# Optimization experiments

Hardware: AMD Instinct MI355X
Metric: run time of the kernel (lower is better)

Reference implementation:

```python
import jax, jax.numpy as jnp
import numpy as np

PATCH = 4   # patch_size
TOPK = 2    # top_k

B, H, W, C = 4, 128, 128, 256
FF, E = 1024, 4


def setup_inputs() -> dict:
    key = jax.random.key(0)
    k1, k2, k3, k4 = jax.random.split(key, 4)
    x = jax.random.normal(k1, (B, H, W, C), dtype=jnp.float32)
    Wg = jax.random.normal(k2, (E, C), dtype=jnp.float32) * 0.01   # router gate (std=0.01 init)
    lim1 = (6.0 / (C + FF)) ** 0.5                                  # xavier_uniform bounds
    W1 = jax.random.uniform(k3, (E, FF, C), minval=-lim1, maxval=lim1, dtype=jnp.float32)
    b1 = jnp.zeros((E, FF), dtype=jnp.float32)
    W2 = jax.random.uniform(k4, (E, C, FF), minval=-lim1, maxval=lim1, dtype=jnp.float32)
    b2 = jnp.zeros((E, C), dtype=jnp.float32)
    return {"x": x, "Wg": Wg, "W1": W1, "b1": b1, "W2": W2, "b2": b2}


def reference(x, Wg, W1, b1, W2, b2):
    Bs, Hs, Ws, Cs = x.shape
    Es = Wg.shape[0]
    ph = pw = PATCH
    nh, nw = Hs // ph, Ws // pw
    P = nh * nw
    # [B, nh, ph, nw, pw, C]
    xp = x.reshape(Bs, nh, ph, nw, pw, Cs)
    # --- router: per-patch avg pool + linear gate ---
    means = xp.mean(axis=(2, 4))                                  # [B, nh, nw, C]
    logits = jnp.einsum('bhwc,ec->bhwe', means, Wg).reshape(Bs, P, Es)
    probs = jax.nn.softmax(logits, axis=-1)
    w, idx = jax.lax.top_k(probs, TOPK)                           # [B, P, K]
    w = w / (w.sum(axis=-1, keepdims=True) + 1e-9)
    # dense combine weights per expert: [B, P, E]
    comb = (jax.nn.one_hot(idx, Es, dtype=w.dtype) * w[..., None]).sum(axis=-2)
    # --- expert dispatch/combine over patch tokens ---
    tokens = xp.transpose(0, 1, 3, 2, 4, 5).reshape(Bs, P, ph * pw, Cs)  # [B,P,T,C]
    out = jnp.zeros_like(tokens)
    for e in range(Es):  # small fixed expert set
        h = jax.nn.gelu(jnp.einsum('bptc,fc->bptf', tokens, W1[e]) + b1[e],
                        approximate=False)
        y = jnp.einsum('bptf,cf->bptc', h, W2[e]) + b2[e]
        out = out + comb[:, :, e, None, None] * y
    # reassemble patches -> [B, H, W, C]
    out = out.reshape(Bs, nh, nw, ph, pw, Cs).transpose(0, 1, 3, 2, 4, 5)
    return out.reshape(Bs, Hs, Ws, Cs)
```

## Files before the change

kernel.cpp:

```cpp
#include <hip/hip_runtime.h>
#include <hip/hip_bf16.h>
#include <cstdint>

#define NB 4
#define NH 128
#define NW 128
#define NC 256
#define NFF 1024
#define NE 4
#define NPATCH 4096
#define NPAIR 16
#define PPB 4
#define BM 64
#define FFC 256

typedef __attribute__((ext_vector_type(8))) short short8;
typedef __attribute__((ext_vector_type(8))) unsigned short ushort8;
typedef __attribute__((ext_vector_type(4))) float f32x4;

__device__ __forceinline__ unsigned short f2b(float f) {
  union { float f; uint32_t u; } v; v.f = f;
  uint32_t u = v.u + 0x7FFFu + ((v.u >> 16) & 1u);
  return (unsigned short)(u >> 16);
}

__device__ __forceinline__ float gelu_f(float v) {
  float u = v * v;
  float t = __builtin_fmaf(u, 0.044715f, 1.0f) * v;
  float e = __builtin_amdgcn_exp2f(t * -2.3022083f);
  return v * __builtin_amdgcn_rcpf(1.0f + e);
}

__device__ __forceinline__ void bar_lgkm() {
  asm volatile("s_waitcnt lgkmcnt(0)" ::: "memory");
  __builtin_amdgcn_s_barrier();
}

__global__ __launch_bounds__(256) void convert_kernel(
    const float* __restrict__ W1, const float* __restrict__ W2,
    unsigned short* __restrict__ W1b, unsigned short* __restrict__ W2b,
    int* __restrict__ cnt, int n) {
  int i = blockIdx.x * blockDim.x + threadIdx.x;
  if (i < NPAIR) cnt[i] = 0;
  if (i < n) {
    W1b[i] = f2b(W1[i]);
    W2b[i] = f2b(W2[i]);
  }
}

__global__ __launch_bounds__(256) void router_kernel(
    const float* __restrict__ x, const float* __restrict__ Wg,
    int* __restrict__ cnt, int* __restrict__ plist, float2* __restrict__ wlist) {
  int p = blockIdx.x;
  int b = p >> 10, pi = p & 1023;
  int phi = pi >> 5, pwi = pi & 31;
  int c = threadIdx.x;

  const float* base = x + (((size_t)(b * NH + phi * 4) * NW) + pwi * 4) * NC + c;
  float s = 0.f;
#pragma unroll
  for (int i = 0; i < 4; i++)
#pragma unroll
    for (int j = 0; j < 4; j++)
      s += base[(i * NW + j) * NC];
  float mean = s * (1.f / 16.f);

  __shared__ float m_lds[NC];
  __shared__ double logit_lds[NE];
  m_lds[c] = mean;
  __syncthreads();

  int wid = c >> 6, lane = c & 63;
  {
    const float* wg = Wg + wid * NC;
    double acc = 0.0;
#pragma unroll
    for (int q = 0; q < 4; q++)
      acc += (double)m_lds[lane + q * 64] * (double)wg[lane + q * 64];
    for (int off = 32; off; off >>= 1) acc += __shfl_down(acc, off);
    if (lane == 0) logit_lds[wid] = acc;
  }
  __syncthreads();

  if (c == 0) {
    double l[NE], pp[NE];
    double mx = -1e300;
#pragma unroll
    for (int i = 0; i < NE; i++) { l[i] = logit_lds[i]; mx = fmax(mx, l[i]); }
    double sum = 0.0;
#pragma unroll
    for (int i = 0; i < NE; i++) { pp[i] = exp(l[i] - mx); sum += pp[i]; }
#pragma unroll
    for (int i = 0; i < NE; i++) pp[i] /= sum;
    int i1 = 0; double p1 = pp[0];
    for (int i = 1; i < NE; i++) if (pp[i] > p1) { p1 = pp[i]; i1 = i; }
    int i2 = -1; double p2 = -1.0;
    for (int i = 0; i < NE; i++) {
      if (i == i1) continue;
      if (pp[i] > p2) { p2 = pp[i]; i2 = i; }
    }
    double den = p1 + p2 + 1e-9;
    float w1 = (float)(p1 / den), w2 = (float)(p2 / den);
    int pr = i1 * NE + i2;
    int pos = atomicAdd(&cnt[pr], 1);
    plist[pr * NPATCH + pos] = p;
    wlist[pr * NPATCH + pos] = make_float2(w1, w2);
  }
}

__global__ __launch_bounds__(256, 2) void ffn_kernel(
    const float* __restrict__ x, const float* __restrict__ b1,
    const float* __restrict__ b2, const unsigned short* __restrict__ W1b,
    const unsigned short* __restrict__ W2b, const int* __restrict__ cnt,
    const int* __restrict__ plist, const float2* __restrict__ wlist,
    float* __restrict__ out) {
  __shared__ unsigned short Xl[BM * NC];
  __shared__ unsigned short Hl[BM * FFC];

  int bid = blockIdx.x;
  int pr = bid & 15;
  int e1 = pr >> 2, e2 = pr & 3;
  int tile = bid >> 4;
  int n = cnt[pr];
  int pbase = tile * PPB;
  if (pbase >= n) return;

  int tid = threadIdx.x, lane = tid & 63, wid = tid >> 6;
  int l15 = lane & 15;
  int kgrp = (lane >> 4) * 8;

  const int*    pl = plist + pr * NPATCH + pbase;
  const float2* wl = wlist + pr * NPATCH + pbase;

  float wvA[PPB], wvB[PPB];
#pragma unroll
  for (int q = 0; q < PPB; q++) {
    if (pbase + q < n) { float2 w = wl[q]; wvA[q] = w.x; wvB[q] = w.y; }
    else { wvA[q] = 0.f; wvB[q] = 0.f; }
  }

  {
    int r  = tid >> 2;
    int c0 = (tid & 3) * 64;
    int pid = (pbase + (r >> 4) < n) ? pl[r >> 4] : -1;
    int t = r & 15;
    if (pid >= 0) {
      int b = pid >> 10, pi = pid & 1023;
      int phi = pi >> 5, pwi = pi & 31;
      const float* src =
          x + (((size_t)(b * NH + phi * 4 + (t >> 2)) * NW) + pwi * 4 + (t & 3)) * NC + c0;
#pragma unroll
      for (int q = 0; q < 8; q++) {
        float4 v0 = *reinterpret_cast<const float4*>(src + q * 8);
        float4 v1 = *reinterpret_cast<const float4*>(src + q * 8 + 4);
        ushort8 h;
        h[0] = f2b(v0.x); h[1] = f2b(v0.y); h[2] = f2b(v0.z); h[3] = f2b(v0.w);
        h[4] = f2b(v1.x); h[5] = f2b(v1.y); h[6] = f2b(v1.z); h[7] = f2b(v1.w);
        int boff = (r * 512 + (c0 + q * 8) * 2) ^ ((r & 7) << 4);
        *reinterpret_cast<ushort8*>((char*)Xl + boff) = h;
      }
    } else {
      ushort8 h = (ushort8)0;
#pragma unroll
      for (int q = 0; q < 8; q++) {
        int boff = (r * 512 + (c0 + q * 8) * 2) ^ ((r & 7) << 4);
        *reinterpret_cast<ushort8*>((char*)Xl + boff) = h;
      }
    }
  }
  bar_lgkm();

  const unsigned short* W1A = W1b + (size_t)e1 * NFF * NC;
  const unsigned short* W1B = W1b + (size_t)e2 * NFF * NC;
  const unsigned short* W2A = W2b + (size_t)e1 * NC * NFF;
  const unsigned short* W2B = W2b + (size_t)e2 * NC * NFF;
  const float* b1A = b1 + e1 * NFF;
  const float* b1B = b1 + e2 * NFF;

  f32x4 acc2[4][4];
#pragma unroll
  for (int a = 0; a < 4; a++)
#pragma unroll
    for (int b = 0; b < 4; b++)
#pragma unroll
      for (int j = 0; j < 4; j++) acc2[a][b][j] = 0.f;

  f32x4 acc1[4][4];
  ushort4 hreg[16];

  auto GEMM1 = [&](const unsigned short* W1e, int fc) {
#pragma unroll
    for (int a = 0; a < 4; a++)
#pragma unroll
      for (int b = 0; b < 4; b++)
#pragma unroll
        for (int j = 0; j < 4; j++) acc1[a][b][j] = 0.f;
#pragma unroll
    for (int ks = 0; ks < 8; ks++) {
      int k = ks * 32 + kgrp;
      short8 bX[4];
#pragma unroll
      for (int nt = 0; nt < 4; nt++) {
        int row = nt * 16 + l15;
        int boff = (row * 512 + k * 2) ^ ((row & 7) << 4);
        bX[nt] = *reinterpret_cast<const short8*>((const char*)Xl + boff);
      }
#pragma unroll
      for (int ftl = 0; ftl < 4; ftl++) {
        int f = fc * FFC + wid * 64 + ftl * 16 + l15;
        short8 aW = *reinterpret_cast<const short8*>(W1e + (size_t)f * NC + k);
#pragma unroll
        for (int nt = 0; nt < 4; nt++)
          acc1[ftl][nt] = __builtin_amdgcn_mfma_f32_16x16x32_bf16(aW, bX[nt], acc1[ftl][nt], 0, 0, 0);
      }
    }
  };

  auto FUSED = [&](const unsigned short* W2p, int fcp,
                   const float* b1e, int fc, bool sideB, bool domfma) {
#pragma unroll
    for (int ks = 0; ks < 8; ks++) {
      if (domfma) {
        int kf = ks * 32 + kgrp;
        short8 aH[4];
#pragma unroll
        for (int rt = 0; rt < 4; rt++) {
          int row = rt * 16 + l15;
          int boff = (row * 512 + kf * 2) ^ ((row & 7) << 4);
          aH[rt] = *reinterpret_cast<const short8*>((const char*)Hl + boff);
        }
#pragma unroll
        for (int ct = 0; ct < 4; ct++) {
          int c = wid * 64 + ct * 16 + l15;
          short8 bW = *reinterpret_cast<const short8*>(W2p + (size_t)c * NFF + fcp * FFC + kf);
#pragma unroll
          for (int rt = 0; rt < 4; rt++)
            acc2[ct][rt] = __builtin_amdgcn_mfma_f32_16x16x32_bf16(aH[rt], bW, acc2[ct][rt], 0, 0, 0);
        }
      }
#pragma unroll
      for (int j = 0; j < 2; j++) {
        int g = ks * 2 + j;
        int ftl = g >> 2, nt = g & 3;
        int f0 = wid * 64 + ftl * 16 + (lane >> 4) * 4;
        float4 bv = *reinterpret_cast<const float4*>(b1e + fc * FFC + f0);
        float w = sideB ? wvB[nt] : wvA[nt];
        ushort4 hp;
        hp.x = f2b(gelu_f(acc1[ftl][nt][0] + bv.x) * w);
        hp.y = f2b(gelu_f(acc1[ftl][nt][1] + bv.y) * w);
        hp.z = f2b(gelu_f(acc1[ftl][nt][2] + bv.z) * w);
        hp.w = f2b(gelu_f(acc1[ftl][nt][3] + bv.w) * w);
        hreg[g] = hp;
      }
    }
  };

  auto WRITEH = [&]() {
#pragma unroll
    for (int g = 0; g < 16; g++) {
      int ftl = g >> 2, nt = g & 3;
      int token = nt * 16 + l15;
      int f0 = wid * 64 + ftl * 16 + (lane >> 4) * 4;
      int boff = (token * 512 + f0 * 2) ^ ((token & 7) << 4);
      *reinterpret_cast<ushort4*>((char*)Hl + boff) = hreg[g];
    }
  };

  GEMM1(W1A, 0);
  FUSED(nullptr, 0, b1A, 0, false, false);
  WRITEH();
  bar_lgkm();

#pragma unroll 1
  for (int i = 1; i < 8; i++) {
    bool sB = (i >= 4);
    int fc = i & 3, fcp = (i - 1) & 3;
    const unsigned short* W1e = sB ? W1B : W1A;
    const float* b1e = sB ? b1B : b1A;
    const unsigned short* W2p = (i - 1 >= 4) ? W2B : W2A;
    GEMM1(W1e, fc);
    FUSED(W2p, fcp, b1e, fc, sB, true);
    bar_lgkm();
    WRITEH();
    bar_lgkm();
  }

  {
#pragma unroll
    for (int ks = 0; ks < 8; ks++) {
      int kf = ks * 32 + kgrp;
      short8 aH[4];
#pragma unroll
      for (int rt = 0; rt < 4; rt++) {
        int row = rt * 16 + l15;
        int boff = (row * 512 + kf * 2) ^ ((row & 7) << 4);
        aH[rt] = *reinterpret_cast<const short8*>((const char*)Hl + boff);
      }
#pragma unroll
      for (int ct = 0; ct < 4; ct++) {
        int c = wid * 64 + ct * 16 + l15;
        short8 bW = *reinterpret_cast<const short8*>(W2B + (size_t)c * NFF + 3 * FFC + kf);
#pragma unroll
        for (int rt = 0; rt < 4; rt++)
          acc2[ct][rt] = __builtin_amdgcn_mfma_f32_16x16x32_bf16(aH[rt], bW, acc2[ct][rt], 0, 0, 0);
      }
    }
  }

  float b2A4[4], b2B4[4];
#pragma unroll
  for (int ct = 0; ct < 4; ct++) {
    int c = wid * 64 + ct * 16 + l15;
    b2A4[ct] = b2[e1 * NC + c];
    b2B4[ct] = b2[e2 * NC + c];
  }
#pragma unroll
  for (int rt = 0; rt < 4; rt++) {
    if (pbase + rt >= n) continue;
    int pid = pl[rt];
    float wA = wvA[rt], wB = wvB[rt];
    int b = pid >> 10, pi = pid & 1023;
    int phi = pi >> 5, pwi = pi & 31;
#pragma unroll
    for (int i2 = 0; i2 < 4; i2++) {
      int t = (lane >> 4) * 4 + i2;
      float* dst =
          out + (((size_t)(b * NH + phi * 4 + (t >> 2)) * NW) + pwi * 4 + (t & 3)) * NC;
#pragma unroll
      for (int ct = 0; ct < 4; ct++) {
        int c = wid * 64 + ct * 16 + l15;
        dst[c] = acc2[ct][rt][i2] + wA * b2A4[ct] + wB * b2B4[ct];
      }
    }
  }
}

extern "C" void kernel_launch(void* const* d_in, const int* in_sizes, int n_in,
                              void* d_out, int out_size, void* d_ws, size_t ws_size,
                              hipStream_t stream) {
  const float* x  = (const float*)d_in[0];
  const float* Wg = (const float*)d_in[1];
  const float* W1 = (const float*)d_in[2];
  const float* b1 = (const float*)d_in[3];
  const float* W2 = (const float*)d_in[4];
  const float* b2 = (const float*)d_in[5];
  float* out = (float*)d_out;

  char* ws = (char*)d_ws;
  unsigned short* W1b = (unsigned short*)ws;
  unsigned short* W2b = (unsigned short*)(ws + (size_t)2 * 1024 * 1024);
  int*    cnt   = (int*)(ws + (size_t)4 * 1024 * 1024);
  int*    plist = (int*)(ws + (size_t)4 * 1024 * 1024 + 256);
  float2* wlist = (float2*)(ws + (size_t)4 * 1024 * 1024 + 256 +
                            (size_t)NPAIR * NPATCH * sizeof(int));

  convert_kernel<<<dim3(4096), dim3(256), 0, stream>>>(W1, W2, W1b, W2b, cnt, NE * NFF * NC);
  router_kernel<<<dim3(NPATCH), dim3(256), 0, stream>>>(x, Wg, cnt, plist, wlist);

  ffn_kernel<<<dim3(NPAIR * (NPATCH / PPB)), dim3(256), 0, stream>>>(
      x, b1, b2, W1b, W2b, cnt, plist, wlist, out);
}
```

Measured before the change: 490.0 us.

## Warp-specialize FFN into producer/consumer waves with double-buffered H and compact worklist

The fused FFN kernel becomes 512-thread blocks. Four waves compute GEMM1 plus GELU into a double-buffered H tile in shared memory, while four other waves consume it for GEMM2, so the two GEMMs overlap through barriers. A new single-block worklist kernel compacts the non-empty (expert-pair, tile) entries, so the FFN grid no longer launches about 16K mostly-empty blocks. MFMA sections are also wrapped in s_setprio. The tighter register budget from launch_bounds(512,2) risks spills in the producer waves.

New measurement: 461.0 us. 5.9% less time.

```diff
diff --git a/kernel.cpp b/kernel.cpp
--- a/kernel.cpp
+++ b/kernel.cpp
@@ -108,40 +108,55 @@
   }
 }
 
-__global__ __launch_bounds__(256, 2) void ffn_kernel(
+__global__ __launch_bounds__(64) void worklist_kernel(
+    const int* __restrict__ cnt, int* __restrict__ wl) {
+  int lane = threadIdx.x;
+  if (lane < NPAIR) {
+    int base = 0, mynb = 0;
+    for (int q = 0; q < NPAIR; ++q) {
+      int nb = (cnt[q] + PPB - 1) / PPB;
+      if (q < lane) base += nb;
+      if (q == lane) mynb = nb;
+    }
+    for (int i = 0; i < mynb; ++i)
+      wl[1 + base + i] = (lane << 12) | (i * PPB);
+    if (lane == NPAIR - 1) wl[0] = base + mynb;
+  }
+}
+
+__global__ __launch_bounds__(512, 2) void ffn_kernel(
     const float* __restrict__ x, const float* __restrict__ b1,
     const float* __restrict__ b2, const unsigned short* __restrict__ W1b,
     const unsigned short* __restrict__ W2b, const int* __restrict__ cnt,
     const int* __restrict__ plist, const float2* __restrict__ wlist,
-    float* __restrict__ out) {
+    const int* __restrict__ wl, float* __restrict__ out) {
   __shared__ unsigned short Xl[BM * NC];
-  __shared__ unsigned short Hl[BM * FFC];
+  __shared__ unsigned short Hl[2][BM * FFC];
 
   int bid = blockIdx.x;
-  int pr = bid & 15;
+  if (bid >= wl[0]) return;
+  int ent = wl[1 + bid];
+  int pr = ent >> 12, pbase = ent & 4095;
   int e1 = pr >> 2, e2 = pr & 3;
-  int tile = bid >> 4;
   int n = cnt[pr];
-  int pbase = tile * PPB;
-  if (pbase >= n) return;
 
   int tid = threadIdx.x, lane = tid & 63, wid = tid >> 6;
   int l15 = lane & 15;
   int kgrp = (lane >> 4) * 8;
 
-  const int*    pl = plist + pr * NPATCH + pbase;
-  const float2* wl = wlist + pr * NPATCH + pbase;
+  const int*    pl  = plist + pr * NPATCH + pbase;
+  const float2* wlp = wlist + pr * NPATCH + pbase;
 
   float wvA[PPB], wvB[PPB];
 #pragma unroll
   for (int q = 0; q < PPB; q++) {
-    if (pbase + q < n) { float2 w = wl[q]; wvA[q] = w.x; wvB[q] = w.y; }
+    if (pbase + q < n) { float2 w = wlp[q]; wvA[q] = w.x; wvB[q] = w.y; }
     else { wvA[q] = 0.f; wvB[q] = 0.f; }
   }
 
   {
-    int r  = tid >> 2;
-    int c0 = (tid & 3) * 64;
+    int r  = tid >> 3;
+    int c0 = (tid & 7) * 32;
     int pid = (pbase + (r >> 4) < n) ? pl[r >> 4] : -1;
     int t = r & 15;
     if (pid >= 0) {
@@ -150,7 +165,7 @@
       const float* src =
           x + (((size_t)(b * NH + phi * 4 + (t >> 2)) * NW) + pwi * 4 + (t & 3)) * NC + c0;
 #pragma unroll
-      for (int q = 0; q < 8; q++) {
+      for (int q = 0; q < 4; q++) {
         float4 v0 = *reinterpret_cast<const float4*>(src + q * 8);
         float4 v1 = *reinterpret_cast<const float4*>(src + q * 8 + 4);
         ushort8 h;
@@ -162,7 +177,7 @@
     } else {
       ushort8 h = (ushort8)0;
 #pragma unroll
-      for (int q = 0; q < 8; q++) {
+      for (int q = 0; q < 4; q++) {
         int boff = (r * 512 + (c0 + q * 8) * 2) ^ ((r & 7) << 4);
         *reinterpret_cast<ushort8*>((char*)Xl + boff) = h;
       }
@@ -170,166 +185,153 @@
   }
   bar_lgkm();
 
-  const unsigned short* W1A = W1b + (size_t)e1 * NFF * NC;
-  const unsigned short* W1B = W1b + (size_t)e2 * NFF * NC;
-  const unsigned short* W2A = W2b + (size_t)e1 * NC * NFF;
-  const unsigned short* W2B = W2b + (size_t)e2 * NC * NFF;
-  const float* b1A = b1 + e1 * NFF;
-  const float* b1B = b1 + e2 * NFF;
-
-  f32x4 acc2[4][4];
-#pragma unroll
-  for (int a = 0; a < 4; a++)
-#pragma unroll
-    for (int b = 0; b < 4; b++)
-#pragma unroll
-      for (int j = 0; j < 4; j++) acc2[a][b][j] = 0.f;
-
-  f32x4 acc1[4][4];
-  ushort4 hreg[16];
-
-  auto GEMM1 = [&](const unsigned short* W1e, int fc) {
+  if (wid < 4) {
+    int wf = wid;
+    const unsigned short* W1A = W1b + (size_t)e1 * NFF * NC;
+    const unsigned short* W1B = W1b + (size_t)e2 * NFF * NC;
+    const float* b1A = b1 + e1 * NFF;
+    const float* b1B = b1 + e2 * NFF;
+
+    f32x4 acc1[4][4];
+    ushort4 hreg[16];
+
+#pragma unroll 1
+    for (int j = 0; j < 8; ++j) {
+      const unsigned short* W1e = (j < 4) ? W1A : W1B;
+      const float* b1e = (j < 4) ? b1A : b1B;
+      int fc = j & 3;
+#pragma unroll
+      for (int a = 0; a < 4; a++)
+#pragma unroll
+        for (int b = 0; b < 4; b++)
+#pragma unroll
+          for (int q = 0; q < 4; q++) acc1[a][b][q] = 0.f;
+
+#pragma unroll
+      for (int ks = 0; ks < 8; ++ks) {
+        int k = ks * 32 + kgrp;
+        short8 bX[4];
+#pragma unroll
+        for (int nt = 0; nt < 4; nt++) {
+          int row = nt * 16 + l15;
+          int boff = (row * 512 + k * 2) ^ ((row & 7) << 4);
+          bX[nt] = *reinterpret_cast<const short8*>((const char*)Xl + boff);
+        }
+        short8 aW[4];
+#pragma unroll
+        for (int ftl = 0; ftl < 4; ftl++) {
+          int f = fc * FFC + wf * 64 + ftl * 16 + l15;
+          aW[ftl] = *reinterpret_cast<const short8*>(W1e + (size_t)f * NC + k);
+        }
+        __builtin_amdgcn_s_setprio(1);
+#pragma unroll
+        for (int ftl = 0; ftl < 4; ftl++)
+#pragma unroll
+          for (int nt = 0; nt < 4; nt++)
+            acc1[ftl][nt] = __builtin_amdgcn_mfma_f32_16x16x32_bf16(
+                aW[ftl], bX[nt], acc1[ftl][nt], 0, 0, 0);
+        __builtin_amdgcn_s_setprio(0);
+      }
+
+#pragma unroll
+      for (int ftl = 0; ftl < 4; ftl++) {
+        int f0 = wf * 64 + ftl * 16 + (lane >> 4) * 4;
+        float4 bv = *reinterpret_cast<const float4*>(b1e + fc * FFC + f0);
+#pragma unroll
+        for (int nt = 0; nt < 4; nt++) {
+          float w = (j < 4) ? wvA[nt] : wvB[nt];
+          ushort4 hp;
+          hp.x = f2b(gelu_f(acc1[ftl][nt][0] + bv.x) * w);
+          hp.y = f2b(gelu_f(acc1[ftl][nt][1] + bv.y) * w);
+          hp.z = f2b(gelu_f(acc1[ftl][nt][2] + bv.z) * w);
+          hp.w = f2b(gelu_f(acc1[ftl][nt][3] + bv.w) * w);
+          hreg[ftl * 4 + nt] = hp;
+        }
+      }
+      unsigned short* Hb = &Hl[j & 1][0];
+#pragma unroll
+      for (int g = 0; g < 16; ++g) {
+        int ftl = g >> 2, nt = g & 3;
+        int token = nt * 16 + l15;
+        int f0 = wf * 64 + ftl * 16 + (lane >> 4) * 4;
+        int boff = (token * 512 + f0 * 2) ^ ((token & 7) << 4);
+        *reinterpret_cast<ushort4*>((char*)Hb + boff) = hreg[g];
+      }
+      bar_lgkm();
+    }
+  } else {
+    int wc = wid - 4;
+    const unsigned short* W2A = W2b + (size_t)e1 * NC * NFF;
+    const unsigned short* W2B = W2b + (size_t)e2 * NC * NFF;
+
+    f32x4 acc2[4][4];
 #pragma unroll
     for (int a = 0; a < 4; a++)
 #pragma unroll
       for (int b = 0; b < 4; b++)
 #pragma unroll
-        for (int j = 0; j < 4; j++) acc1[a][b][j] = 0.f;
-#pragma unroll
-    for (int ks = 0; ks < 8; ks++) {
-      int k = ks * 32 + kgrp;
-      short8 bX[4];
-#pragma unroll
-      for (int nt = 0; nt < 4; nt++) {
-        int row = nt * 16 + l15;
-        int boff = (row * 512 + k * 2) ^ ((row & 7) << 4);
-        bX[nt] = *reinterpret_cast<const short8*>((const char*)Xl + boff);
-      }
-#pragma unroll
-      for (int ftl = 0; ftl < 4; ftl++) {
-        int f = fc * FFC + wid * 64 + ftl * 16 + l15;
-        short8 aW = *reinterpret_cast<const short8*>(W1e + (size_t)f * NC + k);
-#pragma unroll
-        for (int nt = 0; nt < 4; nt++)
-          acc1[ftl][nt] = __builtin_amdgcn_mfma_f32_16x16x32_bf16(aW, bX[nt], acc1[ftl][nt], 0, 0, 0);
-      }
-    }
-  };
-
-  auto FUSED = [&](const unsigned short* W2p, int fcp,
-                   const float* b1e, int fc, bool sideB, bool domfma) {
-#pragma unroll
-    for (int ks = 0; ks < 8; ks++) {
-      if (domfma) {
+        for (int q = 0; q < 4; q++) acc2[a][b][q] = 0.f;
+
+    bar_lgkm();
+
+#pragma unroll 1
+    for (int j = 0; j < 8; ++j) {
+      const unsigned short* W2e = (j < 4) ? W2A : W2B;
+      int fcp = j & 3;
+      const unsigned short* Hb = &Hl[j & 1][0];
+#pragma unroll
+      for (int ks = 0; ks < 8; ++ks) {
         int kf = ks * 32 + kgrp;
         short8 aH[4];
 #pragma unroll
         for (int rt = 0; rt < 4; rt++) {
           int row = rt * 16 + l15;
           int boff = (row * 512 + kf * 2) ^ ((row & 7) << 4);
-          aH[rt] = *reinterpret_cast<const short8*>((const char*)Hl + boff);
-        }
+          aH[rt] = *reinterpret_cast<const short8*>((const char*)Hb + boff);
+        }
+        short8 bW[4];
 #pragma unroll
         for (int ct = 0; ct < 4; ct++) {
-          int c = wid * 64 + ct * 16 + l15;
-          short8 bW = *reinterpret_cast<const short8*>(W2p + (size_t)c * NFF + fcp * FFC + kf);
+          int c = wc * 64 + ct * 16 + l15;
+          bW[ct] = *reinterpret_cast<const short8*>(
+              W2e + (size_t)c * NFF + fcp * FFC + kf);
+        }
+        __builtin_amdgcn_s_setprio(1);
+#pragma unroll
+        for (int ct = 0; ct < 4; ct++)
 #pragma unroll
           for (int rt = 0; rt < 4; rt++)
-            acc2[ct][rt] = __builtin_amdgcn_mfma_f32_16x16x32_bf16(aH[rt], bW, acc2[ct][rt], 0, 0, 0);
-        }
-      }
-#pragma unroll
-      for (int j = 0; j < 2; j++) {
-        int g = ks * 2 + j;
-        int ftl = g >> 2, nt = g & 3;
-        int f0 = wid * 64 + ftl * 16 + (lane >> 4) * 4;
-        float4 bv = *reinterpret_cast<const float4*>(b1e + fc * FFC + f0);
-        float w = sideB ? wvB[nt] : wvA[nt];
-        ushort4 hp;
-        hp.x = f2b(gelu_f(acc1[ftl][nt][0] + bv.x) * w);
-        hp.y = f2b(gelu_f(acc1[ftl][nt][1] + bv.y) * w);
-        hp.z = f2b(gelu_f(acc1[ftl][nt][2] + bv.z) * w);
-        hp.w = f2b(gelu_f(acc1[ftl][nt][3] + bv.w) * w);
-        hreg[g] = hp;
-      }
-    }
-  };
-
-  auto WRITEH = [&]() {
-#pragma unroll
-    for (int g = 0; g < 16; g++) {
-      int ftl = g >> 2, nt = g & 3;
-      int token = nt * 16 + l15;
-      int f0 = wid * 64 + ftl * 16 + (lane >> 4) * 4;
-      int boff = (token * 512 + f0 * 2) ^ ((token & 7) << 4);
-      *reinterpret_cast<ushort4*>((char*)Hl + boff) = hreg[g];
-    }
-  };
-
-  GEMM1(W1A, 0);
-  FUSED(nullptr, 0, b1A, 0, false, false);
-  WRITEH();
-  bar_lgkm();
-
-#pragma unroll 1
-  for (int i = 1; i < 8; i++) {
-    bool sB = (i >= 4);
-    int fc = i & 3, fcp = (i - 1) & 3;
-    const unsigned short* W1e = sB ? W1B : W1A;
-    const float* b1e = sB ? b1B : b1A;
-    const unsigned short* W2p = (i - 1 >= 4) ? W2B : W2A;
-    GEMM1(W1e, fc);
-    FUSED(W2p, fcp, b1e, fc, sB, true);
-    bar_lgkm();
-    WRITEH();
-    bar_lgkm();
-  }
-
-  {
-#pragma unroll
-    for (int ks = 0; ks < 8; ks++) {
-      int kf = ks * 32 + kgrp;
-      short8 aH[4];
-#pragma unroll
-      for (int rt = 0; rt < 4; rt++) {
-        int row = rt * 16 + l15;
-        int boff = (row * 512 + kf * 2) ^ ((row & 7) << 4);
-        aH[rt] = *reinterpret_cast<const short8*>((const char*)Hl + boff);
-      }
-#pragma unroll
-      for (int ct = 0; ct < 4; ct++) {
-        int c = wid * 64 + ct * 16 + l15;
-        short8 bW = *reinterpret_cast<const short8*>(W2B + (size_t)c * NFF + 3 * FFC + kf);
-#pragma unroll
-        for (int rt = 0; rt < 4; rt++)
-          acc2[ct][rt] = __builtin_amdgcn_mfma_f32_16x16x32_bf16(aH[rt], bW, acc2[ct][rt], 0, 0, 0);
-      }
-    }
-  }
-
-  float b2A4[4], b2B4[4];
-#pragma unroll
-  for (int ct = 0; ct < 4; ct++) {
-    int c = wid * 64 + ct * 16 + l15;
-    b2A4[ct] = b2[e1 * NC + c];
-    b2B4[ct] = b2[e2 * NC + c];
-  }
-#pragma unroll
-  for (int rt = 0; rt < 4; rt++) {
-    if (pbase + rt >= n) continue;
-    int pid = pl[rt];
-    float wA = wvA[rt], wB = wvB[rt];
-    int b = pid >> 10, pi = pid & 1023;
-    int phi = pi >> 5, pwi = pi & 31;
-#pragma unroll
-    for (int i2 = 0; i2 < 4; i2++) {
-      int t = (lane >> 4) * 4 + i2;
-      float* dst =
-          out + (((size_t)(b * NH + phi * 4 + (t >> 2)) * NW) + pwi * 4 + (t & 3)) * NC;
-#pragma unroll
-      for (int ct = 0; ct < 4; ct++) {
-        int c = wid * 64 + ct * 16 + l15;
-        dst[c] = acc2[ct][rt][i2] + wA * b2A4[ct] + wB * b2B4[ct];
+            acc2[ct][rt] = __builtin_amdgcn_mfma_f32_16x16x32_bf16(
+                aH[rt], bW[ct], acc2[ct][rt], 0, 0, 0);
+        __builtin_amdgcn_s_setprio(0);
+      }
+      if (j < 7) bar_lgkm();
+    }
+
+    float b2A4[4], b2B4[4];
+#pragma unroll
+    for (int ct = 0; ct < 4; ct++) {
+      int c = wc * 64 + ct * 16 + l15;
+      b2A4[ct] = b2[e1 * NC + c];
+      b2B4[ct] = b2[e2 * NC + c];
+    }
+#pragma unroll
+    for (int rt = 0; rt < 4; rt++) {
+      if (pbase + rt >= n) continue;
+      int pid = pl[rt];
+      float wA = wvA[rt], wB = wvB[rt];
+      int b = pid >> 10, pi = pid & 1023;
+      int phi = pi >> 5, pwi = pi & 31;
+#pragma unroll
+      for (int i2 = 0; i2 < 4; i2++) {
+        int t = (lane >> 4) * 4 + i2;
+        float* dst =
+            out + (((size_t)(b * NH + phi * 4 + (t >> 2)) * NW) + pwi * 4 + (t & 3)) * NC;
+#pragma unroll
+        for (int ct = 0; ct < 4; ct++) {
+          int c = wc * 64 + ct * 16 + l15;
+          dst[c] = acc2[ct][rt][i2] + wA * b2A4[ct] + wB * b2B4[ct];
+        }
       }
     }
   }
@@ -353,10 +355,12 @@
   int*    plist = (int*)(ws + (size_t)4 * 1024 * 1024 + 256);
   float2* wlist = (float2*)(ws + (size_t)4 * 1024 * 1024 + 256 +
                             (size_t)NPAIR * NPATCH * sizeof(int));
+  int*    wl    = (int*)(ws + (size_t)5 * 1024 * 1024);
 
   convert_kernel<<<dim3(4096), dim3(256), 0, stream>>>(W1, W2, W1b, W2b, cnt, NE * NFF * NC);
   router_kernel<<<dim3(NPATCH), dim3(256), 0, stream>>>(x, Wg, cnt, plist, wlist);
-
-  ffn_kernel<<<dim3(NPAIR * (NPATCH / PPB)), dim3(256), 0, stream>>>(
-      x, b1, b2, W1b, W2b, cnt, plist, wlist, out);
-}
+  worklist_kernel<<<dim3(1), dim3(64), 0, stream>>>(cnt, wl);
+
+  ffn_kernel<<<dim3(1040), dim3(512), 0, stream>>>(
+      x, b1, b2, W1b, W2b, cnt, plist, wlist, wl, out);
+}
```
